# Kernel optimization log

Measured on AMD Instinct MI355X. Metric: run time of the kernel, lower is better.

## Reference

```python
import jax, jax.numpy as jnp
import numpy as np

N_NODES = 10000
N_EDGES = 160000
F_IN = 2613
D = 256
H = 4
NEG_SLOPE = 0.2
BN_EPS = 1e-5


def _bn(h, g, b):
    # BatchNorm1d in training mode: batch statistics, biased variance
    return (h - h.mean(0)) / jnp.sqrt(h.var(0) + BN_EPS) * g + b


def _gat_conv(h_in, src, dst, n, W, att_src, att_dst, bias):
    # PyG GATConv, concat=True: h_in [n, F] -> [n, H*D]
    h = (h_in @ W).reshape(n, H, D)                      # [n, H, D]
    a_src = jnp.sum(h * att_src, axis=-1)                # [n, H]
    a_dst = jnp.sum(h * att_dst, axis=-1)                # [n, H]
    e = jax.nn.leaky_relu(a_src[src] + a_dst[dst], NEG_SLOPE)  # [E, H]
    # segment softmax over destination nodes (stable)
    m = jax.ops.segment_max(e, dst, num_segments=n)
    e = jnp.exp(e - m[dst])
    denom = jax.ops.segment_sum(e, dst, num_segments=n)
    alpha = e / (denom[dst] + 1e-16)                     # [E, H]
    out = jax.ops.segment_sum(h[src] * alpha[:, :, None], dst, num_segments=n)
    return out.reshape(n, H * D) + bias


def setup_inputs() -> dict:
    key = jax.random.key(0)
    ks = jax.random.split(key, 24)
    s = 0.02
    inp = {
        "x": jax.random.normal(ks[0], (N_NODES, F_IN), jnp.float32),
        "edges": jax.random.randint(ks[1], (2, N_EDGES), 0, N_NODES, jnp.int64),
        # MLP stack
        "W1": jax.random.normal(ks[2], (F_IN, D), jnp.float32) * s,
        "b1": jnp.zeros((D,), jnp.float32),
        "W2": jax.random.normal(ks[3], (D, D), jnp.float32) * s,
        "b2": jnp.zeros((D,), jnp.float32),
        "W3": jax.random.normal(ks[4], (D, D), jnp.float32) * s,
        "b3": jnp.zeros((D,), jnp.float32),
        # BatchNorm affine params
        "g1": jnp.ones((D,), jnp.float32), "be1": jnp.zeros((D,), jnp.float32),
        "g2": jnp.ones((D,), jnp.float32), "be2": jnp.zeros((D,), jnp.float32),
        "g3": jnp.ones((D,), jnp.float32), "be3": jnp.zeros((D,), jnp.float32),
        "g4": jnp.ones((H * D,), jnp.float32), "be4": jnp.zeros((H * D,), jnp.float32),
        "Wg1": jax.random.normal(ks[5], (D, H * D), jnp.float32) * s,
        "as1": jax.random.normal(ks[6], (H, D), jnp.float32) * s,
        "ad1": jax.random.normal(ks[7], (H, D), jnp.float32) * s,
        "bg1": jnp.zeros((H * D,), jnp.float32),
        "Wg2": jax.random.normal(ks[8], (H * D, H * D), jnp.float32) * s,
        "as2": jax.random.normal(ks[9], (H, D), jnp.float32) * s,
        "ad2": jax.random.normal(ks[10], (H, D), jnp.float32) * s,
        "bg2": jnp.zeros((H * D,), jnp.float32),
    }
    return inp


def reference(x, edges, W1, b1, W2, b2, W3, b3,
              g1, be1, g2, be2, g3, be3, g4, be4,
              Wg1, as1, ad1, bg1, Wg2, as2, ad2, bg2):
    n = x.shape[0]
    src, dst = edges[0], edges[1]
    # PyG: remove existing self-loops then add one per node. We reroute
    # accidental self-loops deterministically, then append self-loops.
    dst = jnp.where(src == dst, (dst + 1) % n, dst)
    loops = jnp.arange(n, dtype=src.dtype)
    src = jnp.concatenate([src, loops])
    dst = jnp.concatenate([dst, loops])

    h = jax.nn.elu(_bn(x @ W1 + b1, g1, be1))
    h = jax.nn.elu(_bn(h @ W2 + b2, g2, be2))
    h = jax.nn.elu(_bn(h @ W3 + b3, g3, be3))
    h = _gat_conv(h, src, dst, n, Wg1, as1, ad1, bg1)
    h = jax.nn.elu(_bn(h, g4, be4))
    h = _gat_conv(h, src, dst, n, Wg2, as2, ad2, bg2)
    return h
```

## Files before the change

### kernel.cpp

```cpp
#include <hip/hip_runtime.h>
#include <hip/hip_bf16.h>

typedef __attribute__((ext_vector_type(8))) short short8v;
typedef __attribute__((ext_vector_type(4))) float f32x4;

__device__ inline float b2f(ushort u) {
  union { uint i; float f; } c;
  c.i = (uint)u << 16;
  return c.f;
}
__device__ inline ushort f2b(float f) {
  __hip_bfloat16 h = __float2bfloat16(f);
  return *(ushort*)&h;
}

template <bool BN, bool ALIGNED>
__global__ __launch_bounds__(256) void gemm_bn(
    const float* __restrict__ A, const __hip_bfloat16* __restrict__ Bh,
    const __hip_bfloat16* __restrict__ Bl, const float* __restrict__ sc,
    const float* __restrict__ sh, float* __restrict__ P, int M, int N, int K,
    int Kp, int nc, int nr, int nz) {
  __shared__ ushort Ash[128][40];
  __shared__ ushort Bsh[128][40];
  __shared__ ushort Asl[128][40];
  __shared__ ushort Bsl[128][40];
  const int nwg = gridDim.x;
  const int b = blockIdx.x;
  const int l = (b & 7) * (nwg >> 3) + (b >> 3);
  const int cb = l % nc;
  const int rr = (l / nc) % nr;
  const int z = l / (nc * nr);

  const int tid = threadIdx.x;
  const int lane = tid & 63;
  const int w = tid >> 6, wr = w >> 1, wc = w & 1;
  const int brow = rr * 128, bcol = cb * 128;
  const int l15 = lane & 15, koff = (lane >> 4) * 8;
  const int arow = tid >> 1, aseg = (tid & 1) * 16;
  const int nK = (K + 31) >> 5;
  const int ks0 = (nK * z) / nz, ks1 = (nK * (z + 1)) / nz;

  f32x4 acc[4][4] = {};

  const int ar = brow + arow;
  const bool arv = ar < M;
  const float* Arow = A + (long)ar * K;
  const __hip_bfloat16* BrowH = Bh + (long)(bcol + arow) * Kp;
  const __hip_bfloat16* BrowL = Bl + (long)(bcol + arow) * Kp;

  for (int ks = ks0; ks < ks1; ++ks) {
    const int k0 = ks << 5;
    const int kbase = k0 + aseg;
    float av[16];
    if (arv) {
      if (ALIGNED) {
        const float4* ap = (const float4*)(Arow + kbase);
#pragma unroll
        for (int q = 0; q < 4; ++q) {
          float4 f = ap[q];
          av[q * 4 + 0] = f.x;
          av[q * 4 + 1] = f.y;
          av[q * 4 + 2] = f.z;
          av[q * 4 + 3] = f.w;
        }
      } else {
        if (kbase + 16 <= K) {
#pragma unroll
          for (int j = 0; j < 16; ++j) av[j] = Arow[kbase + j];
        } else {
#pragma unroll
          for (int j = 0; j < 16; ++j)
            av[j] = (kbase + j < K) ? Arow[kbase + j] : 0.f;
        }
      }
      if (BN) {
#pragma unroll
        for (int q = 0; q < 4; ++q) {
          float4 c4 = *(const float4*)(sc + kbase + q * 4);
          float4 h4 = *(const float4*)(sh + kbase + q * 4);
          float* a4 = &av[q * 4];
          a4[0] = fmaf(a4[0], c4.x, h4.x);
          a4[1] = fmaf(a4[1], c4.y, h4.y);
          a4[2] = fmaf(a4[2], c4.z, h4.z);
          a4[3] = fmaf(a4[3], c4.w, h4.w);
        }
#pragma unroll
        for (int j = 0; j < 16; ++j) {
          float v = av[j];
          av[j] = v > 0.f ? v : (__expf(v) - 1.f);
        }
      }
    } else {
#pragma unroll
      for (int j = 0; j < 16; ++j) av[j] = 0.f;
    }
    short8v ah0, ah1, al0, al1;
#pragma unroll
    for (int j = 0; j < 8; ++j) {
      {
        uint u = __float_as_uint(av[j]);
        ah0[j] = (short)(u >> 16);
        al0[j] = (short)f2b(av[j] - __uint_as_float(u & 0xFFFF0000u));
      }
      {
        uint u = __float_as_uint(av[j + 8]);
        ah1[j] = (short)(u >> 16);
        al1[j] = (short)f2b(av[j + 8] - __uint_as_float(u & 0xFFFF0000u));
      }
    }
    short8v bh0 = *(const short8v*)(BrowH + kbase);
    short8v bh1 = *(const short8v*)(BrowH + kbase + 8);
    short8v bl0 = *(const short8v*)(BrowL + kbase);
    short8v bl1 = *(const short8v*)(BrowL + kbase + 8);
    __syncthreads();
    *(short8v*)&Ash[arow][aseg] = ah0;
    *(short8v*)&Ash[arow][aseg + 8] = ah1;
    *(short8v*)&Bsh[arow][aseg] = bh0;
    *(short8v*)&Bsh[arow][aseg + 8] = bh1;
    *(short8v*)&Asl[arow][aseg] = al0;
    *(short8v*)&Asl[arow][aseg + 8] = al1;
    *(short8v*)&Bsl[arow][aseg] = bl0;
    *(short8v*)&Bsl[arow][aseg + 8] = bl1;
    __syncthreads();

    short8v bfh[4], bfl[4];
#pragma unroll
    for (int nn = 0; nn < 4; ++nn) {
      bfh[nn] = *(const short8v*)&Bsh[wc * 64 + nn * 16 + l15][koff];
      bfl[nn] = *(const short8v*)&Bsl[wc * 64 + nn * 16 + l15][koff];
    }
#pragma unroll
    for (int m = 0; m < 4; ++m) {
      short8v afh = *(const short8v*)&Ash[wr * 64 + m * 16 + l15][koff];
      short8v afl = *(const short8v*)&Asl[wr * 64 + m * 16 + l15][koff];
#pragma unroll
      for (int nn = 0; nn < 4; ++nn) {
        acc[m][nn] = __builtin_amdgcn_mfma_f32_16x16x32_bf16(afh, bfh[nn], acc[m][nn], 0, 0, 0);
        acc[m][nn] = __builtin_amdgcn_mfma_f32_16x16x32_bf16(afh, bfl[nn], acc[m][nn], 0, 0, 0);
        acc[m][nn] = __builtin_amdgcn_mfma_f32_16x16x32_bf16(afl, bfh[nn], acc[m][nn], 0, 0, 0);
      }
    }
  }

  float* outp = P + (long)z * M * N;
#pragma unroll
  for (int m = 0; m < 4; ++m) {
#pragma unroll
    for (int nn = 0; nn < 4; ++nn) {
      int col = bcol + wc * 64 + nn * 16 + l15;
#pragma unroll
      for (int r = 0; r < 4; ++r) {
        int row = brow + wr * 64 + m * 16 + (lane >> 4) * 4 + r;
        if (row < M) outp[(long)row * N + col] = acc[m][nn][r];
      }
    }
  }
}

__global__ __launch_bounds__(256) void gemm_bf16(
    const ushort* __restrict__ A, const __hip_bfloat16* __restrict__ B,
    ushort* __restrict__ C, int M, int N, int K, int nc, int nr) {
  __shared__ ushort Ash[128][40];
  __shared__ ushort Bsh[128][40];
  const int nwg = gridDim.x;
  const int b = blockIdx.x;
  const int l = (b & 7) * (nwg >> 3) + (b >> 3);
  const int cb = l % nc;
  const int rr = l / nc;

  const int tid = threadIdx.x;
  const int lane = tid & 63;
  const int w = tid >> 6, wr = w >> 1, wc = w & 1;
  const int brow = rr * 128, bcol = cb * 128;
  const int l15 = lane & 15, koff = (lane >> 4) * 8;
  const int arow = tid >> 1, aseg = (tid & 1) * 16;
  const int nK = K >> 5;

  f32x4 acc[4][4] = {};
  const short8v zz = {};

  const int ar = brow + arow;
  const bool arv = ar < M;
  const ushort* Arow = A + (long)ar * K;
  const ushort* Brow = (const ushort*)B + (long)(bcol + arow) * K;

  for (int ks = 0; ks < nK; ++ks) {
    const int kbase = (ks << 5) + aseg;
    short8v a0 = arv ? *(const short8v*)(Arow + kbase) : zz;
    short8v a1 = arv ? *(const short8v*)(Arow + kbase + 8) : zz;
    short8v b0 = *(const short8v*)(Brow + kbase);
    short8v b1 = *(const short8v*)(Brow + kbase + 8);
    __syncthreads();
    *(short8v*)&Ash[arow][aseg] = a0;
    *(short8v*)&Ash[arow][aseg + 8] = a1;
    *(short8v*)&Bsh[arow][aseg] = b0;
    *(short8v*)&Bsh[arow][aseg + 8] = b1;
    __syncthreads();

    short8v bf[4];
#pragma unroll
    for (int nn = 0; nn < 4; ++nn)
      bf[nn] = *(const short8v*)&Bsh[wc * 64 + nn * 16 + l15][koff];
#pragma unroll
    for (int m = 0; m < 4; ++m) {
      short8v af = *(const short8v*)&Ash[wr * 64 + m * 16 + l15][koff];
#pragma unroll
      for (int nn = 0; nn < 4; ++nn)
        acc[m][nn] = __builtin_amdgcn_mfma_f32_16x16x32_bf16(af, bf[nn], acc[m][nn], 0, 0, 0);
    }
  }

#pragma unroll
  for (int m = 0; m < 4; ++m) {
#pragma unroll
    for (int nn = 0; nn < 4; ++nn) {
      int col = bcol + wc * 64 + nn * 16 + l15;
#pragma unroll
      for (int r = 0; r < 4; ++r) {
        int row = brow + wr * 64 + m * 16 + (lane >> 4) * 4 + r;
        if (row < M) C[(long)row * N + col] = f2b(acc[m][nn][r]);
      }
    }
  }
}

__global__ __launch_bounds__(256) void bn_elu_b16(
    const float* __restrict__ h, const float* __restrict__ sc,
    const float* __restrict__ sh, ushort* __restrict__ o, long MN, int N) {
  long nq = MN >> 2;
  for (long q = blockIdx.x * 256LL + threadIdx.x; q < nq;
       q += (long)gridDim.x * 256LL) {
    long i = q << 2;
    int col = (int)(i % N);
    float4 v = *(const float4*)(h + i);
    float4 c = *(const float4*)(sc + col);
    float4 s = *(const float4*)(sh + col);
    float a0 = fmaf(v.x, c.x, s.x);
    float a1 = fmaf(v.y, c.y, s.y);
    float a2 = fmaf(v.z, c.z, s.z);
    float a3 = fmaf(v.w, c.w, s.w);
    a0 = a0 > 0.f ? a0 : (__expf(a0) - 1.f);
    a1 = a1 > 0.f ? a1 : (__expf(a1) - 1.f);
    a2 = a2 > 0.f ? a2 : (__expf(a2) - 1.f);
    a3 = a3 > 0.f ? a3 : (__expf(a3) - 1.f);
    ushort4 r;
    r.x = f2b(a0);
    r.y = f2b(a1);
    r.z = f2b(a2);
    r.w = f2b(a3);
    *(ushort4*)(o + i) = r;
  }
}

template <bool BIAS, bool STATS>
__global__ __launch_bounds__(256) void reduce_post(
    const float* __restrict__ P, const float* __restrict__ bias,
    float* __restrict__ C, float* __restrict__ osum, float* __restrict__ osq,
    long MN, int N, int Z) {
  const int col = (int)((blockIdx.x * 256 + threadIdx.x) % N);
  const float bv = BIAS ? bias[col] : 0.f;
  float ps = 0.f, pq = 0.f;
  for (long i = blockIdx.x * 256LL + threadIdx.x; i < MN;
       i += (long)gridDim.x * 256LL) {
    float s = bv;
    for (int zz = 0; zz < Z; ++zz) s += P[(long)zz * MN + i];
    C[i] = s;
    if (STATS) {
      ps += s;
      pq += s * s;
    }
  }
  if (STATS) {
    atomicAdd(&osum[col], ps);
    atomicAdd(&osq[col], pq);
  }
}

__global__ __launch_bounds__(256) void bn_coef(
    const float* __restrict__ ssum, const float* __restrict__ ssq,
    const float* __restrict__ g, const float* __restrict__ be,
    float* __restrict__ sc, float* __restrict__ sh, int N, float invM) {
  int c = blockIdx.x * 256 + threadIdx.x;
  if (c >= N) return;
  float mean = ssum[c] * invM;
  float var = ssq[c] * invM - mean * mean;
  float s = rsqrtf(var + 1e-5f) * g[c];
  sc[c] = s;
  sh[c] = be[c] - mean * s;
}

template <bool LO>
__global__ __launch_bounds__(256) void trans_split(
    const float* __restrict__ W, __hip_bfloat16* __restrict__ Oh,
    __hip_bfloat16* __restrict__ Ol, int K, int N, int Kp) {
  __shared__ float tile[64][65];
  const int k0 = blockIdx.x * 64, n0 = blockIdx.y * 64;
  const int tx = threadIdx.x & 63, ty = threadIdx.x >> 6;
#pragma unroll
  for (int j = 0; j < 16; ++j) {
    int r = ty * 16 + j;
    int k = k0 + r;
    tile[r][tx] = (k < K) ? W[(long)k * N + n0 + tx] : 0.f;
  }
  __syncthreads();
#pragma unroll
  for (int j = 0; j < 16; ++j) {
    int a = ty * 16 + j;
    float v = tile[tx][a];
    long o = (long)(n0 + a) * Kp + k0 + tx;
    if (LO) {
      uint u = __float_as_uint(v);
      ushort hu = (ushort)(u >> 16);
      Oh[o] = *(__hip_bfloat16*)&hu;
      ushort lu = f2b(v - __uint_as_float(u & 0xFFFF0000u));
      Ol[o] = *(__hip_bfloat16*)&lu;
    } else {
      ushort hu = f2b(v);
      Oh[o] = *(__hip_bfloat16*)&hu;
    }
  }
}

__global__ __launch_bounds__(256) void bn_stats(
    const float* __restrict__ h, int M, int N, float* __restrict__ sum,
    float* __restrict__ sumsq) {
  int col = blockIdx.y * 256 + threadIdx.x;
  float s = 0.f, sq = 0.f;
  for (int r = blockIdx.x; r < M; r += gridDim.x) {
    float v = h[(long)r * N + col];
    s += v;
    sq += v * v;
  }
  atomicAdd(&sum[col], s);
  atomicAdd(&sumsq[col], sq);
}

__global__ __launch_bounds__(256) void att_scores_bf16(
    const ushort* __restrict__ hgb, const float* __restrict__ att_s,
    const float* __restrict__ att_d, float* __restrict__ a_src,
    float* __restrict__ a_dst, int n) {
  int node = blockIdx.x;
  int h = threadIdx.x >> 6, lane = threadIdx.x & 63;
  int c = lane * 4;
  ushort4 hv = *(const ushort4*)(hgb + (long)node * 1024 + h * 256 + c);
  float4 as = *(const float4*)(att_s + h * 256 + c);
  float4 ad = *(const float4*)(att_d + h * 256 + c);
  float x0 = b2f(hv.x), x1 = b2f(hv.y), x2 = b2f(hv.z), x3 = b2f(hv.w);
  float ss = x0 * as.x + x1 * as.y + x2 * as.z + x3 * as.w;
  float sd = x0 * ad.x + x1 * ad.y + x2 * ad.z + x3 * ad.w;
#pragma unroll
  for (int off = 32; off; off >>= 1) {
    ss += __shfl_down(ss, off);
    sd += __shfl_down(sd, off);
  }
  if (lane == 0) {
    a_src[node * 4 + h] = ss;
    a_dst[node * 4 + h] = sd;
  }
}

__global__ __launch_bounds__(256) void deg_count(
    const int* __restrict__ srcA, const int* __restrict__ dstA,
    int* __restrict__ deg, int n, int E0, int E) {
  int e = blockIdx.x * blockDim.x + threadIdx.x;
  if (e >= E) return;
  int d;
  if (e < E0) {
    int s = srcA[e];
    d = dstA[e];
    if (s == d) d = (d + 1) % n;
  } else {
    d = e - E0;
  }
  atomicAdd(&deg[d], 1);
}

__global__ __launch_bounds__(256) void scan_rows(
    const int* __restrict__ deg, int* __restrict__ row_start, int n) {
  __shared__ int sums[256];
  int t = threadIdx.x;
  int chunk = (n + 255) / 256;
  int start = t * chunk, end = min(start + chunk, n);
  int s = 0;
  for (int i = start; i < end; ++i) s += deg[i];
  sums[t] = s;
  __syncthreads();
  for (int off = 1; off < 256; off <<= 1) {
    int v = (t >= off) ? sums[t - off] : 0;
    __syncthreads();
    sums[t] += v;
    __syncthreads();
  }
  int run = (t == 0) ? 0 : sums[t - 1];
  for (int i = start; i < end; ++i) {
    row_start[i] = run;
    run += deg[i];
  }
  if (t == 255) row_start[n] = run;
}

__global__ __launch_bounds__(256) void scatter_edges(
    const int* __restrict__ srcA, const int* __restrict__ dstA,
    int* __restrict__ cursor, int* __restrict__ csr_src, int n, int E0, int E) {
  int e = blockIdx.x * blockDim.x + threadIdx.x;
  if (e >= E) return;
  int s, d;
  if (e < E0) {
    s = srcA[e];
    d = dstA[e];
    if (s == d) d = (d + 1) % n;
  } else {
    s = d = e - E0;
  }
  int pos = atomicAdd(&cursor[d], 1);
  csr_src[pos] = s;
}

__global__ __launch_bounds__(256) void aggregate_fused(
    const ushort* __restrict__ hgb, const int* __restrict__ row_start,
    const int* __restrict__ csr_src, const float* __restrict__ a_src,
    const float* __restrict__ a_dst, const float* __restrict__ bias,
    float* __restrict__ out) {
  int d = blockIdx.x;
  int t = threadIdx.x;
  int hh = t >> 6;
  int off = hh * 256 + (t & 63) * 4;
  int p0 = row_start[d], p1 = row_start[d + 1];
  float adv = a_dst[d * 4 + hh];
  float den = 1e-16f;
  float4 acc = {0.f, 0.f, 0.f, 0.f};
  for (int p = p0; p < p1; ++p) {
    int s = csr_src[p];
    float v = a_src[s * 4 + hh] + adv;
    v = v > 0.f ? v : 0.2f * v;
    float ex = __expf(v);
    den += ex;
    ushort4 hv = *(const ushort4*)(hgb + (long)s * 1024 + off);
    acc.x += ex * b2f(hv.x);
    acc.y += ex * b2f(hv.y);
    acc.z += ex * b2f(hv.z);
    acc.w += ex * b2f(hv.w);
  }
  float rden = 1.f / den;
  float4 bv = *(const float4*)(bias + off);
  float4 o;
  o.x = bv.x + acc.x * rden;
  o.y = bv.y + acc.y * rden;
  o.z = bv.z + acc.z * rden;
  o.w = bv.w + acc.w * rden;
  *(float4*)(out + (long)d * 1024 + off) = o;
}

extern "C" void kernel_launch(void* const* d_in, const int* in_sizes, int n_in,
                              void* d_out, int out_size, void* d_ws,
                              size_t ws_size, hipStream_t stream) {
  const float* x = (const float*)d_in[0];
  const int* edges = (const int*)d_in[1];
  const float* W1 = (const float*)d_in[2];
  const float* b1 = (const float*)d_in[3];
  const float* W2 = (const float*)d_in[4];
  const float* b2 = (const float*)d_in[5];
  const float* W3 = (const float*)d_in[6];
  const float* b3 = (const float*)d_in[7];
  const float* g1 = (const float*)d_in[8];
  const float* be1 = (const float*)d_in[9];
  const float* g2 = (const float*)d_in[10];
  const float* be2 = (const float*)d_in[11];
  const float* g3 = (const float*)d_in[12];
  const float* be3 = (const float*)d_in[13];
  const float* g4 = (const float*)d_in[14];
  const float* be4 = (const float*)d_in[15];
  const float* Wg1 = (const float*)d_in[16];
  const float* as1 = (const float*)d_in[17];
  const float* ad1 = (const float*)d_in[18];
  const float* bg1 = (const float*)d_in[19];
  const float* Wg2 = (const float*)d_in[20];
  const float* as2 = (const float*)d_in[21];
  const float* ad2 = (const float*)d_in[22];
  const float* bg2 = (const float*)d_in[23];
  float* out = (float*)d_out;

  const int n = 10000, E0 = 160000, E = 170000;
  const int F = 2613, Fp = 2624, D = 256, HD = 1024;
  const int* srcA = edges;
  const int* dstA = edges + E0;

  uint8_t* p = (uint8_t*)d_ws;
  auto alloc = [&](size_t bytes) -> void* {
    void* r = (void*)p;
    p += (bytes + 255) & ~(size_t)255;
    return r;
  };
  float* h1 = (float*)alloc((size_t)n * D * 4);
  float* h2 = (float*)alloc((size_t)n * D * 4);
  float* h3 = (float*)alloc((size_t)n * D * 4);
  float* agg = (float*)alloc((size_t)n * HD * 4);
  float* pbuf = (float*)alloc((size_t)8 * n * D * 4);
  ushort* hgb = (ushort*)alloc((size_t)n * HD * 2);
  ushort* actb = (ushort*)alloc((size_t)n * HD * 2);
  __hip_bfloat16* W1h = (__hip_bfloat16*)alloc((size_t)D * Fp * 2);
  __hip_bfloat16* W1l = (__hip_bfloat16*)alloc((size_t)D * Fp * 2);
  __hip_bfloat16* W2h = (__hip_bfloat16*)alloc((size_t)D * D * 2);
  __hip_bfloat16* W2l = (__hip_bfloat16*)alloc((size_t)D * D * 2);
  __hip_bfloat16* W3h = (__hip_bfloat16*)alloc((size_t)D * D * 2);
  __hip_bfloat16* W3l = (__hip_bfloat16*)alloc((size_t)D * D * 2);
  __hip_bfloat16* Wg1h = (__hip_bfloat16*)alloc((size_t)HD * D * 2);
  __hip_bfloat16* Wg2h = (__hip_bfloat16*)alloc((size_t)HD * HD * 2);
  float* asrc = (float*)alloc((size_t)n * 4 * 4);
  float* adst = (float*)alloc((size_t)n * 4 * 4);
  float* sc1 = (float*)alloc(D * 4);
  float* sh1 = (float*)alloc(D * 4);
  float* sc2 = (float*)alloc(D * 4);
  float* sh2 = (float*)alloc(D * 4);
  float* sc3 = (float*)alloc(D * 4);
  float* sh3 = (float*)alloc(D * 4);
  float* sc4 = (float*)alloc(HD * 4);
  float* sh4 = (float*)alloc(HD * 4);
  int* row_start = (int*)alloc((size_t)(n + 1) * 4);
  int* cursor = (int*)alloc((size_t)n * 4);
  int* csr_src = (int*)alloc((size_t)E * 4);
  uint8_t* z0 = p;
  float* ssum1 = (float*)alloc(D * 4);
  float* ssq1 = (float*)alloc(D * 4);
  float* ssum2 = (float*)alloc(D * 4);
  float* ssq2 = (float*)alloc(D * 4);
  float* ssum3 = (float*)alloc(D * 4);
  float* ssq3 = (float*)alloc(D * 4);
  float* ssum4 = (float*)alloc(HD * 4);
  float* ssq4 = (float*)alloc(HD * 4);
  int* deg = (int*)alloc((size_t)n * 4);
  size_t zbytes = (size_t)(p - z0);

  dim3 blk(256);
  const int rb = (n + 127) / 128;
  const int eb = (E + 255) / 256;
  const long MN_D = (long)n * D;
  const long MN_HD = (long)n * HD;
  const float invM = 1.f / (float)n;
  const int gL1 = 2 * rb * 8;
  const int gMLP = 2 * rb * 4;
  const int gGAT = 8 * rb;

  hipMemsetAsync(z0, 0, zbytes, stream);

  deg_count<<<eb, blk, 0, stream>>>(srcA, dstA, deg, n, E0, E);
  scan_rows<<<1, blk, 0, stream>>>(deg, row_start, n);
  hipMemcpyAsync(cursor, row_start, n * sizeof(int), hipMemcpyDeviceToDevice, stream);
  scatter_edges<<<eb, blk, 0, stream>>>(srcA, dstA, cursor, csr_src, n, E0, E);

  trans_split<true><<<dim3(Fp / 64, D / 64), blk, 0, stream>>>(W1, W1h, W1l, F, D, Fp);
  trans_split<true><<<dim3(D / 64, D / 64), blk, 0, stream>>>(W2, W2h, W2l, D, D, D);
  trans_split<true><<<dim3(D / 64, D / 64), blk, 0, stream>>>(W3, W3h, W3l, D, D, D);
  trans_split<false><<<dim3(D / 64, HD / 64), blk, 0, stream>>>(Wg1, Wg1h, nullptr, D, HD, D);
  trans_split<false><<<dim3(HD / 64, HD / 64), blk, 0, stream>>>(Wg2, Wg2h, nullptr, HD, HD, HD);

  gemm_bn<false, false><<<gL1, blk, 0, stream>>>(
      x, W1h, W1l, nullptr, nullptr, pbuf, n, D, F, Fp, 2, rb, 8);
  reduce_post<true, true><<<512, blk, 0, stream>>>(pbuf, b1, h1, ssum1, ssq1, MN_D, D, 8);
  bn_coef<<<1, blk, 0, stream>>>(ssum1, ssq1, g1, be1, sc1, sh1, D, invM);

  gemm_bn<true, true><<<gMLP, blk, 0, stream>>>(
      h1, W2h, W2l, sc1, sh1, pbuf, n, D, D, D, 2, rb, 4);
  reduce_post<true, true><<<512, blk, 0, stream>>>(pbuf, b2, h2, ssum2, ssq2, MN_D, D, 4);
  bn_coef<<<1, blk, 0, stream>>>(ssum2, ssq2, g2, be2, sc2, sh2, D, invM);

  gemm_bn<true, true><<<gMLP, blk, 0, stream>>>(
      h2, W3h, W3l, sc2, sh2, pbuf, n, D, D, D, 2, rb, 4);
  reduce_post<true, true><<<512, blk, 0, stream>>>(pbuf, b3, h3, ssum3, ssq3, MN_D, D, 4);
  bn_coef<<<1, blk, 0, stream>>>(ssum3, ssq3, g3, be3, sc3, sh3, D, invM);

  bn_elu_b16<<<1024, blk, 0, stream>>>(h3, sc3, sh3, actb, MN_D, D);
  gemm_bf16<<<gGAT, blk, 0, stream>>>(actb, Wg1h, hgb, n, HD, D, 8, rb);
  att_scores_bf16<<<n, blk, 0, stream>>>(hgb, as1, ad1, asrc, adst, n);
  aggregate_fused<<<n, blk, 0, stream>>>(hgb, row_start, csr_src, asrc, adst, bg1, agg);

  bn_stats<<<dim3(64, HD / 256), blk, 0, stream>>>(agg, n, HD, ssum4, ssq4);
  bn_coef<<<4, blk, 0, stream>>>(ssum4, ssq4, g4, be4, sc4, sh4, HD, invM);
  bn_elu_b16<<<2048, blk, 0, stream>>>(agg, sc4, sh4, actb, MN_HD, HD);

  gemm_bf16<<<gGAT, blk, 0, stream>>>(actb, Wg2h, hgb, n, HD, HD, 8, rb);
  att_scores_bf16<<<n, blk, 0, stream>>>(hgb, as2, ad2, asrc, adst, n);
  aggregate_fused<<<n, blk, 0, stream>>>(hgb, row_start, csr_src, asrc, adst, bg2, out);
}
```

Baseline: 572.7 us.

## Load GEMM B and bf16 A tiles directly from global memory into LDS

Replaces the register-staged global-to-shared copies of the B tiles in the split-bf16 GEMM, and of both A and B tiles in the bf16 GEMM, with 16-byte global_load_lds transfers. The shared tiles become unpadded 128x32 arrays filled contiguously, four 8-element segments per row. This removes the register round-trip and the ds_write instructions, which should cut VGPR use and issue slots. In exchange, the unpadded layout may cause LDS bank conflicts on the MFMA fragment reads. The bf16 GEMM also drops the row bound check on A, so the last partial row tile reads past M.

Result: no change. 572.8 us (+0.0%).

```diff
diff --git a/kernel.cpp b/kernel.cpp
--- a/kernel.cpp
+++ b/kernel.cpp
@@ -12,6 +12,12 @@
 __device__ inline ushort f2b(float f) {
   __hip_bfloat16 h = __float2bfloat16(f);
   return *(ushort*)&h;
+}
+
+typedef __attribute__((address_space(1))) const unsigned int guint;
+typedef __attribute__((address_space(3))) unsigned int luint;
+__device__ __forceinline__ void gload16(const void* g, void* l) {
+  __builtin_amdgcn_global_load_lds((guint*)g, (luint*)l, 16, 0, 0);
 }
 
 template <bool BN, bool ALIGNED>
@@ -21,9 +27,9 @@
     const float* __restrict__ sh, float* __restrict__ P, int M, int N, int K,
     int Kp, int nc, int nr, int nz) {
   __shared__ ushort Ash[128][40];
-  __shared__ ushort Bsh[128][40];
   __shared__ ushort Asl[128][40];
-  __shared__ ushort Bsl[128][40];
+  __shared__ ushort Bs2[128][32];
+  __shared__ ushort Bl2[128][32];
   const int nwg = gridDim.x;
   const int b = blockIdx.x;
   const int l = (b & 7) * (nwg >> 3) + (b >> 3);
@@ -37,6 +43,7 @@
   const int brow = rr * 128, bcol = cb * 128;
   const int l15 = lane & 15, koff = (lane >> 4) * 8;
   const int arow = tid >> 1, aseg = (tid & 1) * 16;
+  const int srow = tid >> 2, sseg = (tid & 3) * 8;
   const int nK = (K + 31) >> 5;
   const int ks0 = (nK * z) / nz, ks1 = (nK * (z + 1)) / nz;
 
@@ -45,8 +52,14 @@
   const int ar = brow + arow;
   const bool arv = ar < M;
   const float* Arow = A + (long)ar * K;
-  const __hip_bfloat16* BrowH = Bh + (long)(bcol + arow) * Kp;
-  const __hip_bfloat16* BrowL = Bl + (long)(bcol + arow) * Kp;
+  const ushort* gBh0 = (const ushort*)Bh + (long)(bcol + srow) * Kp + sseg;
+  const ushort* gBh1 = (const ushort*)Bh + (long)(bcol + 64 + srow) * Kp + sseg;
+  const ushort* gBl0 = (const ushort*)Bl + (long)(bcol + srow) * Kp + sseg;
+  const ushort* gBl1 = (const ushort*)Bl + (long)(bcol + 64 + srow) * Kp + sseg;
+  ushort* lBh0 = &Bs2[0][0] + ((w * 64) << 3);
+  ushort* lBh1 = &Bs2[0][0] + ((256 + w * 64) << 3);
+  ushort* lBl0 = &Bl2[0][0] + ((w * 64) << 3);
+  ushort* lBl1 = &Bl2[0][0] + ((256 + w * 64) << 3);
 
   for (int ks = ks0; ks < ks1; ++ks) {
     const int k0 = ks << 5;
@@ -108,26 +121,22 @@
         al1[j] = (short)f2b(av[j + 8] - __uint_as_float(u & 0xFFFF0000u));
       }
     }
-    short8v bh0 = *(const short8v*)(BrowH + kbase);
-    short8v bh1 = *(const short8v*)(BrowH + kbase + 8);
-    short8v bl0 = *(const short8v*)(BrowL + kbase);
-    short8v bl1 = *(const short8v*)(BrowL + kbase + 8);
     __syncthreads();
+    gload16(gBh0 + k0, lBh0);
+    gload16(gBh1 + k0, lBh1);
+    gload16(gBl0 + k0, lBl0);
+    gload16(gBl1 + k0, lBl1);
     *(short8v*)&Ash[arow][aseg] = ah0;
     *(short8v*)&Ash[arow][aseg + 8] = ah1;
-    *(short8v*)&Bsh[arow][aseg] = bh0;
-    *(short8v*)&Bsh[arow][aseg + 8] = bh1;
     *(short8v*)&Asl[arow][aseg] = al0;
     *(short8v*)&Asl[arow][aseg + 8] = al1;
-    *(short8v*)&Bsl[arow][aseg] = bl0;
-    *(short8v*)&Bsl[arow][aseg + 8] = bl1;
     __syncthreads();
 
     short8v bfh[4], bfl[4];
 #pragma unroll
     for (int nn = 0; nn < 4; ++nn) {
-      bfh[nn] = *(const short8v*)&Bsh[wc * 64 + nn * 16 + l15][koff];
-      bfl[nn] = *(const short8v*)&Bsl[wc * 64 + nn * 16 + l15][koff];
+      bfh[nn] = *(const short8v*)&Bs2[wc * 64 + nn * 16 + l15][koff];
+      bfl[nn] = *(const short8v*)&Bl2[wc * 64 + nn * 16 + l15][koff];
     }
 #pragma unroll
     for (int m = 0; m < 4; ++m) {
@@ -160,8 +169,8 @@
 __global__ __launch_bounds__(256) void gemm_bf16(
     const ushort* __restrict__ A, const __hip_bfloat16* __restrict__ B,
     ushort* __restrict__ C, int M, int N, int K, int nc, int nr) {
-  __shared__ ushort Ash[128][40];
-  __shared__ ushort Bsh[128][40];
+  __shared__ ushort A2[128][32];
+  __shared__ ushort B2[128][32];
   const int nwg = gridDim.x;
   const int b = blockIdx.x;
   const int l = (b & 7) * (nwg >> 3) + (b >> 3);
@@ -173,37 +182,36 @@
   const int w = tid >> 6, wr = w >> 1, wc = w & 1;
   const int brow = rr * 128, bcol = cb * 128;
   const int l15 = lane & 15, koff = (lane >> 4) * 8;
-  const int arow = tid >> 1, aseg = (tid & 1) * 16;
+  const int srow = tid >> 2, sseg = (tid & 3) * 8;
   const int nK = K >> 5;
 
   f32x4 acc[4][4] = {};
-  const short8v zz = {};
-
-  const int ar = brow + arow;
-  const bool arv = ar < M;
-  const ushort* Arow = A + (long)ar * K;
-  const ushort* Brow = (const ushort*)B + (long)(bcol + arow) * K;
+
+  const ushort* gA0 = A + (long)(brow + srow) * K + sseg;
+  const ushort* gA1 = A + (long)(brow + 64 + srow) * K + sseg;
+  const ushort* gB0 = (const ushort*)B + (long)(bcol + srow) * K + sseg;
+  const ushort* gB1 = (const ushort*)B + (long)(bcol + 64 + srow) * K + sseg;
+  ushort* lA0 = &A2[0][0] + ((w * 64) << 3);
+  ushort* lA1 = &A2[0][0] + ((256 + w * 64) << 3);
+  ushort* lB0 = &B2[0][0] + ((w * 64) << 3);
+  ushort* lB1 = &B2[0][0] + ((256 + w * 64) << 3);
 
   for (int ks = 0; ks < nK; ++ks) {
-    const int kbase = (ks << 5) + aseg;
-    short8v a0 = arv ? *(const short8v*)(Arow + kbase) : zz;
-    short8v a1 = arv ? *(const short8v*)(Arow + kbase + 8) : zz;
-    short8v b0 = *(const short8v*)(Brow + kbase);
-    short8v b1 = *(const short8v*)(Brow + kbase + 8);
+    const int k0 = ks << 5;
     __syncthreads();
-    *(short8v*)&Ash[arow][aseg] = a0;
-    *(short8v*)&Ash[arow][aseg + 8] = a1;
-    *(short8v*)&Bsh[arow][aseg] = b0;
-    *(short8v*)&Bsh[arow][aseg + 8] = b1;
+    gload16(gA0 + k0, lA0);
+    gload16(gA1 + k0, lA1);
+    gload16(gB0 + k0, lB0);
+    gload16(gB1 + k0, lB1);
     __syncthreads();
 
     short8v bf[4];
 #pragma unroll
     for (int nn = 0; nn < 4; ++nn)
-      bf[nn] = *(const short8v*)&Bsh[wc * 64 + nn * 16 + l15][koff];
+      bf[nn] = *(const short8v*)&B2[wc * 64 + nn * 16 + l15][koff];
 #pragma unroll
     for (int m = 0; m < 4; ++m) {
-      short8v af = *(const short8v*)&Ash[wr * 64 + m * 16 + l15][koff];
+      short8v af = *(const short8v*)&A2[wr * 64 + m * 16 + l15][koff];
 #pragma unroll
       for (int nn = 0; nn < 4; ++nn)
         acc[m][nn] = __builtin_amdgcn_mfma_f32_16x16x32_bf16(af, bf[nn], acc[m][nn], 0, 0, 0);
```
